# Optimization experiments

Measured on AMD Instinct MI355X. Metric: run time of the kernel, lower is better.

Reference implementation:

```python
import jax, jax.numpy as jnp
import numpy as np

N_NODES = 50000
N_EDGES = 800000
F_IN = 128
HIDDEN = 128
N_CLASSES = 40


def setup_inputs() -> dict:
    key = jax.random.key(0)
    k1, k2, k3, k4 = jax.random.split(key, 4)
    features = jax.random.normal(k1, (N_NODES, F_IN), dtype=jnp.float32)
    edge_index = jax.random.randint(k2, (2, N_EDGES), 0, N_NODES, dtype=jnp.int64)
    # Glorot-style init for the GCNConv linear weights, zero bias (PyG default)
    W1 = jax.random.normal(k3, (F_IN, HIDDEN), dtype=jnp.float32) * (1.0 / np.sqrt(F_IN))
    b1 = jnp.zeros((HIDDEN,), dtype=jnp.float32)
    W2 = jax.random.normal(k4, (HIDDEN, N_CLASSES), dtype=jnp.float32) * (1.0 / np.sqrt(HIDDEN))
    b2 = jnp.zeros((N_CLASSES,), dtype=jnp.float32)
    return {"features": features, "edge_index": edge_index,
            "W1": W1, "b1": b1, "W2": W2, "b2": b2}


def _gcn_norm(edge_index, num_nodes):
    # Add self-loops and compute symmetric normalization D^-1/2 (A+I) D^-1/2
    loop = jnp.arange(num_nodes, dtype=edge_index.dtype)
    src = jnp.concatenate([edge_index[0], loop])  # [E+N]
    dst = jnp.concatenate([edge_index[1], loop])  # [E+N]
    w = jnp.ones(src.shape[0], dtype=jnp.float32)
    deg = jax.ops.segment_sum(w, dst, num_segments=num_nodes)  # [N]
    dinv = jnp.where(deg > 0, jax.lax.rsqrt(deg), 0.0)
    norm = dinv[src] * w * dinv[dst]  # [E+N]
    return src, dst, norm


def _gcn_conv(x, W, b, src, dst, norm, num_nodes):
    h = x @ W  # linear transform first (PyG GCNConv): [N, out]
    msg = h[src] * norm[:, None]  # gather + scale: [E+N, out]
    out = jax.ops.segment_sum(msg, dst, num_segments=num_nodes)  # scatter-add
    return out + b


def reference(features, edge_index, W1, b1, W2, b2):
    n = features.shape[0]
    src, dst, norm = _gcn_norm(edge_index, n)
    x = jax.nn.relu(_gcn_conv(features, W1, b1, src, dst, norm, n))
    # dropout is identity at eval time (training=False)
    x = _gcn_conv(x, W2, b2, src, dst, norm, n)
    return jax.nn.log_softmax(x, axis=1)
```

## Files before the change

### kernel.cpp

```cpp
#include <hip/hip_runtime.h>
#include <hip/hip_bf16.h>
#include <math.h>

#define N_NODES 50000
#define N_EDGES 800000

#define SCAN_CHUNK 512
#define SCAN_NB ((N_NODES + SCAN_CHUNK - 1) / SCAN_CHUNK)

__global__ __launch_bounds__(256) void count_kernel(const int* __restrict__ ei,
                                                    int* __restrict__ cnt) {
  int e = blockIdx.x * 256 + threadIdx.x;
  if (e < N_EDGES) {
    int d = ei[N_EDGES + e];
    d = min(max(d, 0), N_NODES - 1);
    atomicAdd(&cnt[d], 1);
  }
}

__global__ __launch_bounds__(256) void scan_reduce(const int* __restrict__ cnt,
                                                   int* __restrict__ bsum) {
  __shared__ int s[256];
  int t = threadIdx.x;
  int i0 = blockIdx.x * SCAN_CHUNK + t * 2;
  int v = 0;
  if (i0 < N_NODES) v += cnt[i0];
  if (i0 + 1 < N_NODES) v += cnt[i0 + 1];
  s[t] = v;
  __syncthreads();
  for (int off = 128; off > 0; off >>= 1) {
    if (t < off) s[t] += s[t + off];
    __syncthreads();
  }
  if (t == 0) bsum[blockIdx.x] = s[0];
}

__global__ void scan_block(int* bsum) {
  __shared__ int s[128];
  int t = threadIdx.x;
  int v = (t < SCAN_NB) ? bsum[t] : 0;
  s[t] = v;
  __syncthreads();
  for (int off = 1; off < 128; off <<= 1) {
    int a = (t >= off) ? s[t - off] : 0;
    __syncthreads();
    s[t] += a;
    __syncthreads();
  }
  if (t < SCAN_NB) bsum[t] = s[t] - v;
}

__global__ __launch_bounds__(256) void scan_final(const int* __restrict__ cnt,
                                                  const int* __restrict__ bsum,
                                                  int* __restrict__ rowptr,
                                                  int* __restrict__ cursor,
                                                  float* __restrict__ dinv) {
  __shared__ int s[256];
  int t = threadIdx.x;
  int b = blockIdx.x;
  int i0 = b * SCAN_CHUNK + t * 2;
  int c0 = (i0 < N_NODES) ? cnt[i0] : 0;
  int c1 = (i0 + 1 < N_NODES) ? cnt[i0 + 1] : 0;
  int v = c0 + c1;
  s[t] = v;
  __syncthreads();
  for (int off = 1; off < 256; off <<= 1) {
    int a = (t >= off) ? s[t - off] : 0;
    __syncthreads();
    s[t] += a;
    __syncthreads();
  }
  int excl = s[t] - v + bsum[b];
  if (i0 < N_NODES) {
    rowptr[i0] = excl;
    cursor[i0] = excl;
    dinv[i0] = rsqrtf((float)(c0 + 1));
  }
  if (i0 + 1 < N_NODES) {
    rowptr[i0 + 1] = excl + c0;
    cursor[i0 + 1] = excl + c0;
    dinv[i0 + 1] = rsqrtf((float)(c1 + 1));
  }
  if (b == 0 && t == 0) rowptr[N_NODES] = N_EDGES;
}

__global__ __launch_bounds__(256) void fill_kernel(const int* __restrict__ ei,
                                                   int* __restrict__ cursor,
                                                   int* __restrict__ col) {
  int e = blockIdx.x * 256 + threadIdx.x;
  if (e >= N_EDGES) return;
  int srcv = ei[e];
  int dstv = ei[N_EDGES + e];
  srcv = min(max(srcv, 0), N_NODES - 1);
  dstv = min(max(dstv, 0), N_NODES - 1);
  int p = atomicAdd(&cursor[dstv], 1);
  col[p] = srcv;
}

__global__ __launch_bounds__(256) void gemm1_kernel(const float* __restrict__ X,
                                                    const float* __restrict__ W,
                                                    const float* __restrict__ dinv,
                                                    float* __restrict__ h1p) {
  __shared__ float xs[128 * 64];
  __shared__ float ws[128 * 64];
  int t = threadIdx.x;
  int row0 = blockIdx.x * 128;
  int wv = t >> 6, lane = t & 63;
  int wr = (wv >> 1) << 6, wc = (wv & 1) << 6;
  int tr = lane >> 3, tc = lane & 7;
  float acc[8][8];
#pragma unroll
  for (int i = 0; i < 8; ++i)
#pragma unroll
    for (int m = 0; m < 8; ++m) acc[i][m] = 0.f;

  for (int h = 0; h < 2; ++h) {
    if (h) __syncthreads();
#pragma unroll
    for (int it = 0; it < 8; ++it) {
      int idx = t + it * 256;
      int r = idx >> 4, kq = idx & 15;
      int gr = row0 + r;
      if (gr >= N_NODES) gr = N_NODES - 1;
      float4 v = *(const float4*)(X + (size_t)gr * 128 + h * 64 + kq * 4);
      *(float4*)(xs + r * 64 + ((kq ^ (r & 7)) << 2)) = v;
    }
#pragma unroll
    for (int it = 0; it < 8; ++it) {
      int idx = t + it * 256;
      int k = idx >> 5, jq = idx & 31;
      float4 v = *(const float4*)(W + (size_t)(h * 64 + k) * 128 + jq * 4);
      int kc = k >> 2, kr = k & 3;
      int j0 = jq * 4;
      ws[(j0 + 0) * 64 + (((kc ^ ((j0 + 0) & 7)) << 2) | kr)] = v.x;
      ws[(j0 + 1) * 64 + (((kc ^ ((j0 + 1) & 7)) << 2) | kr)] = v.y;
      ws[(j0 + 2) * 64 + (((kc ^ ((j0 + 2) & 7)) << 2) | kr)] = v.z;
      ws[(j0 + 3) * 64 + (((kc ^ ((j0 + 3) & 7)) << 2) | kr)] = v.w;
    }
    __syncthreads();
    for (int kq = 0; kq < 16; ++kq) {
      float4 xv[8], wvv[8];
#pragma unroll
      for (int i = 0; i < 8; ++i)
        xv[i] = *(const float4*)(xs + (wr + tr + 8 * i) * 64 + ((kq ^ tr) << 2));
#pragma unroll
      for (int m = 0; m < 8; ++m)
        wvv[m] = *(const float4*)(ws + (wc + tc + 8 * m) * 64 + ((kq ^ tc) << 2));
#pragma unroll
      for (int i = 0; i < 8; ++i)
#pragma unroll
        for (int m = 0; m < 8; ++m) {
          acc[i][m] = fmaf(xv[i].x, wvv[m].x, acc[i][m]);
          acc[i][m] = fmaf(xv[i].y, wvv[m].y, acc[i][m]);
          acc[i][m] = fmaf(xv[i].z, wvv[m].z, acc[i][m]);
          acc[i][m] = fmaf(xv[i].w, wvv[m].w, acc[i][m]);
        }
    }
  }
#pragma unroll
  for (int i = 0; i < 8; ++i) {
    int gr = row0 + wr + tr + 8 * i;
    if (gr < N_NODES) {
      float di = dinv[gr];
#pragma unroll
      for (int m = 0; m < 8; ++m)
        h1p[(size_t)gr * 128 + wc + tc + 8 * m] = di * acc[i][m];
    }
  }
}

__global__ __launch_bounds__(256) void agg1_kernel(const float* __restrict__ h1p,
                                                   const int* __restrict__ rowptr,
                                                   const int* __restrict__ col,
                                                   const float* __restrict__ dinv,
                                                   const float* __restrict__ b1,
                                                   float* __restrict__ x2) {
  int wid = (blockIdx.x * 256 + threadIdx.x) >> 6;
  int lane = threadIdx.x & 63;
  if (wid >= N_NODES) return;
  int rs = rowptr[wid], re = rowptr[wid + 1];
  int half = lane >> 5;
  int fl = lane & 31;
  const float4* hp4 = (const float4*)h1p;
  float4 z = {0.f, 0.f, 0.f, 0.f};
  float4 a0 = (half == 0) ? hp4[(size_t)wid * 32 + fl] : z;
  float4 a1 = z, a2 = z, a3 = z;
  for (int base = rs; base < re; base += 64) {
    int idx = base + lane;
    int c = (idx < re) ? col[idx] : 0;
    int nb = min(64, re - base);
    int e = 0;
    for (; e + 8 <= nb; e += 8) {
      int s0 = __shfl(c, e + half);
      int s1 = __shfl(c, e + 2 + half);
      int s2 = __shfl(c, e + 4 + half);
      int s3 = __shfl(c, e + 6 + half);
      float4 v0 = hp4[(size_t)s0 * 32 + fl];
      float4 v1 = hp4[(size_t)s1 * 32 + fl];
      float4 v2 = hp4[(size_t)s2 * 32 + fl];
      float4 v3 = hp4[(size_t)s3 * 32 + fl];
      a0.x += v0.x; a0.y += v0.y; a0.z += v0.z; a0.w += v0.w;
      a1.x += v1.x; a1.y += v1.y; a1.z += v1.z; a1.w += v1.w;
      a2.x += v2.x; a2.y += v2.y; a2.z += v2.z; a2.w += v2.w;
      a3.x += v3.x; a3.y += v3.y; a3.z += v3.z; a3.w += v3.w;
    }
    for (; e + 2 <= nb; e += 2) {
      int s0 = __shfl(c, e + half);
      float4 v0 = hp4[(size_t)s0 * 32 + fl];
      a0.x += v0.x; a0.y += v0.y; a0.z += v0.z; a0.w += v0.w;
    }
    if (e < nb) {
      int s0 = __shfl(c, e);
      if (half == 0) {
        float4 v0 = hp4[(size_t)s0 * 32 + fl];
        a0.x += v0.x; a0.y += v0.y; a0.z += v0.z; a0.w += v0.w;
      }
    }
  }
  float4 a;
  a.x = (a0.x + a1.x) + (a2.x + a3.x);
  a.y = (a0.y + a1.y) + (a2.y + a3.y);
  a.z = (a0.z + a1.z) + (a2.z + a3.z);
  a.w = (a0.w + a1.w) + (a2.w + a3.w);
  a.x += __shfl_xor(a.x, 32);
  a.y += __shfl_xor(a.y, 32);
  a.z += __shfl_xor(a.z, 32);
  a.w += __shfl_xor(a.w, 32);
  if (half == 0) {
    float di = dinv[wid];
    float4 bb = ((const float4*)b1)[fl];
    float4 o;
    o.x = fmaxf(fmaf(di, a.x, bb.x), 0.f);
    o.y = fmaxf(fmaf(di, a.y, bb.y), 0.f);
    o.z = fmaxf(fmaf(di, a.z, bb.z), 0.f);
    o.w = fmaxf(fmaf(di, a.w, bb.w), 0.f);
    *(float4*)(x2 + (size_t)wid * 128 + fl * 4) = o;
  }
}

__global__ __launch_bounds__(256) void gemm2_kernel(const float* __restrict__ X2,
                                                    const float* __restrict__ W2,
                                                    const float* __restrict__ dinv,
                                                    float* __restrict__ h2p) {
  __shared__ float xs[64 * 128];
  __shared__ float ws[40 * 128];
  int t = threadIdx.x;
  int row0 = blockIdx.x * 64;
#pragma unroll
  for (int it = 0; it < 8; ++it) {
    int idx = t + it * 256;
    int r = idx >> 5, kq = idx & 31;
    int gr = row0 + r;
    if (gr >= N_NODES) gr = N_NODES - 1;
    float4 v = *(const float4*)(X2 + (size_t)gr * 128 + kq * 4);
    *(float4*)(xs + r * 128 + ((kq ^ (r & 7)) << 2)) = v;
  }
  for (int idx = t; idx < 1280; idx += 256) {
    int k = idx / 10, jq = idx % 10;
    float4 v = *(const float4*)(W2 + k * 40 + jq * 4);
    int kc = k >> 2, kr = k & 3;
    int j0 = jq * 4;
    ws[(j0 + 0) * 128 + (((kc ^ ((j0 + 0) & 7)) << 2) | kr)] = v.x;
    ws[(j0 + 1) * 128 + (((kc ^ ((j0 + 1) & 7)) << 2) | kr)] = v.y;
    ws[(j0 + 2) * 128 + (((kc ^ ((j0 + 2) & 7)) << 2) | kr)] = v.z;
    ws[(j0 + 3) * 128 + (((kc ^ ((j0 + 3) & 7)) << 2) | kr)] = v.w;
  }
  __syncthreads();
  int wv = t >> 6, lane = t & 63;
  int tr = lane >> 3, tc = lane & 7;
  int rbase = wv * 16;
  float acc[2][5];
#pragma unroll
  for (int i = 0; i < 2; ++i)
#pragma unroll
    for (int m = 0; m < 5; ++m) acc[i][m] = 0.f;
  for (int kq = 0; kq < 32; ++kq) {
    float4 xv[2], wvv[5];
#pragma unroll
    for (int i = 0; i < 2; ++i)
      xv[i] = *(const float4*)(xs + (rbase + tr + 8 * i) * 128 + ((kq ^ tr) << 2));
#pragma unroll
    for (int m = 0; m < 5; ++m)
      wvv[m] = *(const float4*)(ws + (tc + 8 * m) * 128 + ((kq ^ tc) << 2));
#pragma unroll
    for (int i = 0; i < 2; ++i)
#pragma unroll
      for (int m = 0; m < 5; ++m) {
        acc[i][m] = fmaf(xv[i].x, wvv[m].x, acc[i][m]);
        acc[i][m] = fmaf(xv[i].y, wvv[m].y, acc[i][m]);
        acc[i][m] = fmaf(xv[i].z, wvv[m].z, acc[i][m]);
        acc[i][m] = fmaf(xv[i].w, wvv[m].w, acc[i][m]);
      }
  }
#pragma unroll
  for (int i = 0; i < 2; ++i) {
    int gr = row0 + rbase + tr + 8 * i;
    if (gr < N_NODES) {
      float di = dinv[gr];
#pragma unroll
      for (int m = 0; m < 5; ++m)
        h2p[(size_t)gr * 40 + tc + 8 * m] = di * acc[i][m];
    }
  }
}

__global__ __launch_bounds__(256) void agg2_softmax_kernel(const float* __restrict__ h2p,
                                                           const int* __restrict__ rowptr,
                                                           const int* __restrict__ col,
                                                           const float* __restrict__ dinv,
                                                           const float* __restrict__ b2,
                                                           float* __restrict__ out) {
  int wid = (blockIdx.x * 256 + threadIdx.x) >> 6;
  int lane = threadIdx.x & 63;
  if (wid >= N_NODES) return;
  int rs = rowptr[wid], re = rowptr[wid + 1];
  bool act = lane < 40;
  float ac0 = act ? h2p[(size_t)wid * 40 + lane] : 0.f;
  float ac1 = 0.f, ac2 = 0.f, ac3 = 0.f;
  for (int base = rs; base < re; base += 64) {
    int idx = base + lane;
    int c = (idx < re) ? col[idx] : 0;
    int nb = min(64, re - base);
    int e = 0;
    for (; e + 4 <= nb; e += 4) {
      int s0 = __shfl(c, e), s1 = __shfl(c, e + 1);
      int s2 = __shfl(c, e + 2), s3 = __shfl(c, e + 3);
      if (act) {
        ac0 += h2p[(size_t)s0 * 40 + lane];
        ac1 += h2p[(size_t)s1 * 40 + lane];
        ac2 += h2p[(size_t)s2 * 40 + lane];
        ac3 += h2p[(size_t)s3 * 40 + lane];
      }
    }
    for (; e < nb; ++e) {
      int s0 = __shfl(c, e);
      if (act) ac0 += h2p[(size_t)s0 * 40 + lane];
    }
  }
  float acc = (ac0 + ac1) + (ac2 + ac3);
  float v = act ? fmaf(dinv[wid], acc, b2[lane]) : -1e30f;
  float m = v;
#pragma unroll
  for (int off = 32; off > 0; off >>= 1) m = fmaxf(m, __shfl_xor(m, off));
  float ex = act ? expf(v - m) : 0.f;
  float ssum = ex;
#pragma unroll
  for (int off = 32; off > 0; off >>= 1) ssum += __shfl_xor(ssum, off);
  float ls = logf(ssum);
  if (act) out[(size_t)wid * 40 + lane] = v - m - ls;
}

extern "C" void kernel_launch(void* const* d_in, const int* in_sizes, int n_in,
                              void* d_out, int out_size, void* d_ws, size_t ws_size,
                              hipStream_t stream) {
  const float* X = (const float*)d_in[0];
  const int* ei = (const int*)d_in[1];
  const float* W1 = (const float*)d_in[2];
  const float* b1 = (const float*)d_in[3];
  const float* W2 = (const float*)d_in[4];
  const float* b2 = (const float*)d_in[5];
  float* out = (float*)d_out;

  char* p = (char*)d_ws;
  auto carve = [&](size_t bytes) -> void* {
    void* q = (void*)p;
    p += (bytes + 255) & ~(size_t)255;
    return q;
  };
  float* h1p = (float*)carve((size_t)N_NODES * 128 * 4);
  float* x2 = (float*)carve((size_t)N_NODES * 128 * 4);
  float* h2p = (float*)carve((size_t)N_NODES * 40 * 4);
  int* col = (int*)carve((size_t)N_EDGES * 4);
  int* cnt = (int*)carve((size_t)N_NODES * 4);
  int* rowptr = (int*)carve((size_t)(N_NODES + 1) * 4);
  int* cursor = (int*)carve((size_t)N_NODES * 4);
  float* dinv = (float*)carve((size_t)N_NODES * 4);
  int* bsum = (int*)carve((size_t)SCAN_NB * 4);

  hipMemsetAsync(cnt, 0, (size_t)N_NODES * 4, stream);
  count_kernel<<<(N_EDGES + 255) / 256, 256, 0, stream>>>(ei, cnt);
  scan_reduce<<<SCAN_NB, 256, 0, stream>>>(cnt, bsum);
  scan_block<<<1, 128, 0, stream>>>(bsum);
  scan_final<<<SCAN_NB, 256, 0, stream>>>(cnt, bsum, rowptr, cursor, dinv);
  fill_kernel<<<(N_EDGES + 255) / 256, 256, 0, stream>>>(ei, cursor, col);
  gemm1_kernel<<<(N_NODES + 127) / 128, 256, 0, stream>>>(X, W1, dinv, h1p);
  agg1_kernel<<<(N_NODES + 3) / 4, 256, 0, stream>>>(h1p, rowptr, col, dinv, b1, x2);
  gemm2_kernel<<<(N_NODES + 63) / 64, 256, 0, stream>>>(x2, W2, dinv, h2p);
  agg2_softmax_kernel<<<(N_NODES + 3) / 4, 256, 0, stream>>>(h2p, rowptr, col, dinv, b2, out);
}
```

Measured before the change: 314.4 us.

## Fuse CSR construction into one cooperative kernel and pad h2p rows to 48

Replaces the memset and the five CSR-building kernels (count, scan_reduce, scan_block, scan_final, fill) with one cooperative kernel of 256 blocks. Its phases are separated by grid-wide syncs, and the scan now covers one node per thread. This removes several launch gaps and the separate memset at the cost of grid-barrier overhead and fewer threads running the atomic count and fill loops. It also pads the layer-2 feature rows from 40 to 48 floats, so each gathered row starts on a 64-byte boundary and touches fewer cache lines during aggregation.

```diff
diff --git a/kernel.cpp b/kernel.cpp
--- a/kernel.cpp
+++ b/kernel.cpp
@@ -1,67 +1,40 @@
 #include <hip/hip_runtime.h>
 #include <hip/hip_bf16.h>
+#include <hip/hip_cooperative_groups.h>
 #include <math.h>
+
+namespace cg = cooperative_groups;
 
 #define N_NODES 50000
 #define N_EDGES 800000
 
-#define SCAN_CHUNK 512
-#define SCAN_NB ((N_NODES + SCAN_CHUNK - 1) / SCAN_CHUNK)
-
-__global__ __launch_bounds__(256) void count_kernel(const int* __restrict__ ei,
-                                                    int* __restrict__ cnt) {
-  int e = blockIdx.x * 256 + threadIdx.x;
-  if (e < N_EDGES) {
+#define CSR_NB 256
+
+__global__ __launch_bounds__(256) void coop_csr_kernel(const int* __restrict__ ei,
+                                                       int* __restrict__ cnt,
+                                                       int* __restrict__ bsum,
+                                                       int* __restrict__ rowptr,
+                                                       int* __restrict__ cursor,
+                                                       float* __restrict__ dinv,
+                                                       int* __restrict__ col) {
+  cg::grid_group grid = cg::this_grid();
+  __shared__ int s[256];
+  int t = threadIdx.x;
+  int bid = blockIdx.x;
+  int tid = bid * 256 + t;
+  const int NT = CSR_NB * 256;
+
+  for (int i = tid; i < N_NODES; i += NT) cnt[i] = 0;
+  grid.sync();
+
+  for (int e = tid; e < N_EDGES; e += NT) {
     int d = ei[N_EDGES + e];
     d = min(max(d, 0), N_NODES - 1);
     atomicAdd(&cnt[d], 1);
   }
-}
-
-__global__ __launch_bounds__(256) void scan_reduce(const int* __restrict__ cnt,
-                                                   int* __restrict__ bsum) {
-  __shared__ int s[256];
-  int t = threadIdx.x;
-  int i0 = blockIdx.x * SCAN_CHUNK + t * 2;
-  int v = 0;
-  if (i0 < N_NODES) v += cnt[i0];
-  if (i0 + 1 < N_NODES) v += cnt[i0 + 1];
-  s[t] = v;
-  __syncthreads();
-  for (int off = 128; off > 0; off >>= 1) {
-    if (t < off) s[t] += s[t + off];
-    __syncthreads();
-  }
-  if (t == 0) bsum[blockIdx.x] = s[0];
-}
-
-__global__ void scan_block(int* bsum) {
-  __shared__ int s[128];
-  int t = threadIdx.x;
-  int v = (t < SCAN_NB) ? bsum[t] : 0;
-  s[t] = v;
-  __syncthreads();
-  for (int off = 1; off < 128; off <<= 1) {
-    int a = (t >= off) ? s[t - off] : 0;
-    __syncthreads();
-    s[t] += a;
-    __syncthreads();
-  }
-  if (t < SCAN_NB) bsum[t] = s[t] - v;
-}
-
-__global__ __launch_bounds__(256) void scan_final(const int* __restrict__ cnt,
-                                                  const int* __restrict__ bsum,
-                                                  int* __restrict__ rowptr,
-                                                  int* __restrict__ cursor,
-                                                  float* __restrict__ dinv) {
-  __shared__ int s[256];
-  int t = threadIdx.x;
-  int b = blockIdx.x;
-  int i0 = b * SCAN_CHUNK + t * 2;
-  int c0 = (i0 < N_NODES) ? cnt[i0] : 0;
-  int c1 = (i0 + 1 < N_NODES) ? cnt[i0 + 1] : 0;
-  int v = c0 + c1;
+  grid.sync();
+
+  int v = (tid < N_NODES) ? cnt[tid] : 0;
   s[t] = v;
   __syncthreads();
   for (int off = 1; off < 256; off <<= 1) {
@@ -70,31 +43,42 @@
     s[t] += a;
     __syncthreads();
   }
-  int excl = s[t] - v + bsum[b];
-  if (i0 < N_NODES) {
-    rowptr[i0] = excl;
-    cursor[i0] = excl;
-    dinv[i0] = rsqrtf((float)(c0 + 1));
-  }
-  if (i0 + 1 < N_NODES) {
-    rowptr[i0 + 1] = excl + c0;
-    cursor[i0 + 1] = excl + c0;
-    dinv[i0 + 1] = rsqrtf((float)(c1 + 1));
-  }
-  if (b == 0 && t == 0) rowptr[N_NODES] = N_EDGES;
-}
-
-__global__ __launch_bounds__(256) void fill_kernel(const int* __restrict__ ei,
-                                                   int* __restrict__ cursor,
-                                                   int* __restrict__ col) {
-  int e = blockIdx.x * 256 + threadIdx.x;
-  if (e >= N_EDGES) return;
-  int srcv = ei[e];
-  int dstv = ei[N_EDGES + e];
-  srcv = min(max(srcv, 0), N_NODES - 1);
-  dstv = min(max(dstv, 0), N_NODES - 1);
-  int p = atomicAdd(&cursor[dstv], 1);
-  col[p] = srcv;
+  int incl = s[t];
+  int excl = incl - v;
+  if (t == 255) bsum[bid] = incl;
+  grid.sync();
+
+  if (bid == 0) {
+    int b = bsum[t];
+    s[t] = b;
+    __syncthreads();
+    for (int off = 1; off < 256; off <<= 1) {
+      int a = (t >= off) ? s[t - off] : 0;
+      __syncthreads();
+      s[t] += a;
+      __syncthreads();
+    }
+    bsum[t] = s[t] - b;
+  }
+  grid.sync();
+
+  if (tid < N_NODES) {
+    int e0 = excl + bsum[bid];
+    rowptr[tid] = e0;
+    cursor[tid] = e0;
+    dinv[tid] = rsqrtf((float)(v + 1));
+  }
+  if (tid == 0) rowptr[N_NODES] = N_EDGES;
+  grid.sync();
+
+  for (int e = tid; e < N_EDGES; e += NT) {
+    int srcv = ei[e];
+    int dstv = ei[N_EDGES + e];
+    srcv = min(max(srcv, 0), N_NODES - 1);
+    dstv = min(max(dstv, 0), N_NODES - 1);
+    int p = atomicAdd(&cursor[dstv], 1);
+    col[p] = srcv;
+  }
 }
 
 __global__ __launch_bounds__(256) void gemm1_kernel(const float* __restrict__ X,
@@ -299,7 +283,7 @@
       float di = dinv[gr];
 #pragma unroll
       for (int m = 0; m < 5; ++m)
-        h2p[(size_t)gr * 40 + tc + 8 * m] = di * acc[i][m];
+        h2p[(size_t)gr * 48 + tc + 8 * m] = di * acc[i][m];
     }
   }
 }
@@ -315,7 +299,7 @@
   if (wid >= N_NODES) return;
   int rs = rowptr[wid], re = rowptr[wid + 1];
   bool act = lane < 40;
-  float ac0 = act ? h2p[(size_t)wid * 40 + lane] : 0.f;
+  float ac0 = act ? h2p[(size_t)wid * 48 + lane] : 0.f;
   float ac1 = 0.f, ac2 = 0.f, ac3 = 0.f;
   for (int base = rs; base < re; base += 64) {
     int idx = base + lane;
@@ -326,15 +310,15 @@
       int s0 = __shfl(c, e), s1 = __shfl(c, e + 1);
       int s2 = __shfl(c, e + 2), s3 = __shfl(c, e + 3);
       if (act) {
-        ac0 += h2p[(size_t)s0 * 40 + lane];
-        ac1 += h2p[(size_t)s1 * 40 + lane];
-        ac2 += h2p[(size_t)s2 * 40 + lane];
-        ac3 += h2p[(size_t)s3 * 40 + lane];
+        ac0 += h2p[(size_t)s0 * 48 + lane];
+        ac1 += h2p[(size_t)s1 * 48 + lane];
+        ac2 += h2p[(size_t)s2 * 48 + lane];
+        ac3 += h2p[(size_t)s3 * 48 + lane];
       }
     }
     for (; e < nb; ++e) {
       int s0 = __shfl(c, e);
-      if (act) ac0 += h2p[(size_t)s0 * 40 + lane];
+      if (act) ac0 += h2p[(size_t)s0 * 48 + lane];
     }
   }
   float acc = (ac0 + ac1) + (ac2 + ac3);
@@ -369,20 +353,18 @@
   };
   float* h1p = (float*)carve((size_t)N_NODES * 128 * 4);
   float* x2 = (float*)carve((size_t)N_NODES * 128 * 4);
-  float* h2p = (float*)carve((size_t)N_NODES * 40 * 4);
+  float* h2p = (float*)carve((size_t)N_NODES * 48 * 4);
   int* col = (int*)carve((size_t)N_EDGES * 4);
   int* cnt = (int*)carve((size_t)N_NODES * 4);
   int* rowptr = (int*)carve((size_t)(N_NODES + 1) * 4);
   int* cursor = (int*)carve((size_t)N_NODES * 4);
   float* dinv = (float*)carve((size_t)N_NODES * 4);
-  int* bsum = (int*)carve((size_t)SCAN_NB * 4);
-
-  hipMemsetAsync(cnt, 0, (size_t)N_NODES * 4, stream);
-  count_kernel<<<(N_EDGES + 255) / 256, 256, 0, stream>>>(ei, cnt);
-  scan_reduce<<<SCAN_NB, 256, 0, stream>>>(cnt, bsum);
-  scan_block<<<1, 128, 0, stream>>>(bsum);
-  scan_final<<<SCAN_NB, 256, 0, stream>>>(cnt, bsum, rowptr, cursor, dinv);
-  fill_kernel<<<(N_EDGES + 255) / 256, 256, 0, stream>>>(ei, cursor, col);
+  int* bsum = (int*)carve((size_t)CSR_NB * 4);
+
+  void* csr_args[] = {(void*)&ei, (void*)&cnt, (void*)&bsum, (void*)&rowptr,
+                      (void*)&cursor, (void*)&dinv, (void*)&col};
+  hipLaunchCooperativeKernel((const void*)coop_csr_kernel, dim3(CSR_NB), dim3(256),
+                             csr_args, 0, stream);
   gemm1_kernel<<<(N_NODES + 127) / 128, 256, 0, stream>>>(X, W1, dinv, h1p);
   agg1_kernel<<<(N_NODES + 3) / 4, 256, 0, stream>>>(h1p, rowptr, col, dinv, b1, x2);
   gemm2_kernel<<<(N_NODES + 63) / 64, 256, 0, stream>>>(x2, W2, dinv, h2p);
```

New measurement: 469.0 us. +49.2%, slower.

## Store first-layer hidden features in bf16 and pad second-layer rows to 48

Applied to the files above, without the earlier changes.

The first GEMM now writes its normalized output as bf16, which halves the bytes the first aggregation gathers per neighbor. The aggregation kernel is restructured so each quarter-wave handles one neighbor row with 16 lanes loading 8 bf16 values each, and bf16 is unpacked to fp32 with shifts and masks before accumulating. The second-layer intermediate row stride is padded from 40 to 48 floats, which aligns gathered rows. Rounding to bf16 adds accuracy loss to the hidden activations.

```diff
diff --git a/kernel.cpp b/kernel.cpp
--- a/kernel.cpp
+++ b/kernel.cpp
@@ -100,7 +100,7 @@
 __global__ __launch_bounds__(256) void gemm1_kernel(const float* __restrict__ X,
                                                     const float* __restrict__ W,
                                                     const float* __restrict__ dinv,
-                                                    float* __restrict__ h1p) {
+                                                    __hip_bfloat16* __restrict__ h1p) {
   __shared__ float xs[128 * 64];
   __shared__ float ws[128 * 64];
   int t = threadIdx.x;
@@ -164,12 +164,12 @@
       float di = dinv[gr];
 #pragma unroll
       for (int m = 0; m < 8; ++m)
-        h1p[(size_t)gr * 128 + wc + tc + 8 * m] = di * acc[i][m];
-    }
-  }
-}
-
-__global__ __launch_bounds__(256) void agg1_kernel(const float* __restrict__ h1p,
+        h1p[(size_t)gr * 128 + wc + tc + 8 * m] = __float2bfloat16(di * acc[i][m]);
+    }
+  }
+}
+
+__global__ __launch_bounds__(256) void agg1_kernel(const __hip_bfloat16* __restrict__ h1p,
                                                    const int* __restrict__ rowptr,
                                                    const int* __restrict__ col,
                                                    const float* __restrict__ dinv,
@@ -179,62 +179,72 @@
   int lane = threadIdx.x & 63;
   if (wid >= N_NODES) return;
   int rs = rowptr[wid], re = rowptr[wid + 1];
-  int half = lane >> 5;
-  int fl = lane & 31;
-  const float4* hp4 = (const float4*)h1p;
-  float4 z = {0.f, 0.f, 0.f, 0.f};
-  float4 a0 = (half == 0) ? hp4[(size_t)wid * 32 + fl] : z;
-  float4 a1 = z, a2 = z, a3 = z;
+  int q = lane >> 4;
+  int fl = lane & 15;
+  const uint4* hp = (const uint4*)h1p;
+  float a0[8], a1[8];
+#pragma unroll
+  for (int j = 0; j < 8; ++j) { a0[j] = 0.f; a1[j] = 0.f; }
+
+#define ACC_BF16(A, U)                                                        \
+  {                                                                           \
+    uint4 u_ = (U);                                                           \
+    A[0] += __uint_as_float(u_.x << 16);                                      \
+    A[1] += __uint_as_float(u_.x & 0xffff0000u);                              \
+    A[2] += __uint_as_float(u_.y << 16);                                      \
+    A[3] += __uint_as_float(u_.y & 0xffff0000u);                              \
+    A[4] += __uint_as_float(u_.z << 16);                                      \
+    A[5] += __uint_as_float(u_.z & 0xffff0000u);                              \
+    A[6] += __uint_as_float(u_.w << 16);                                      \
+    A[7] += __uint_as_float(u_.w & 0xffff0000u);                              \
+  }
+
+  if (q == 0) ACC_BF16(a0, hp[(size_t)wid * 16 + fl]);
+
   for (int base = rs; base < re; base += 64) {
     int idx = base + lane;
     int c = (idx < re) ? col[idx] : 0;
     int nb = min(64, re - base);
     int e = 0;
     for (; e + 8 <= nb; e += 8) {
-      int s0 = __shfl(c, e + half);
-      int s1 = __shfl(c, e + 2 + half);
-      int s2 = __shfl(c, e + 4 + half);
-      int s3 = __shfl(c, e + 6 + half);
-      float4 v0 = hp4[(size_t)s0 * 32 + fl];
-      float4 v1 = hp4[(size_t)s1 * 32 + fl];
-      float4 v2 = hp4[(size_t)s2 * 32 + fl];
-      float4 v3 = hp4[(size_t)s3 * 32 + fl];
-      a0.x += v0.x; a0.y += v0.y; a0.z += v0.z; a0.w += v0.w;
-      a1.x += v1.x; a1.y += v1.y; a1.z += v1.z; a1.w += v1.w;
-      a2.x += v2.x; a2.y += v2.y; a2.z += v2.z; a2.w += v2.w;
-      a3.x += v3.x; a3.y += v3.y; a3.z += v3.z; a3.w += v3.w;
-    }
-    for (; e + 2 <= nb; e += 2) {
-      int s0 = __shfl(c, e + half);
-      float4 v0 = hp4[(size_t)s0 * 32 + fl];
-      a0.x += v0.x; a0.y += v0.y; a0.z += v0.z; a0.w += v0.w;
-    }
-    if (e < nb) {
-      int s0 = __shfl(c, e);
-      if (half == 0) {
-        float4 v0 = hp4[(size_t)s0 * 32 + fl];
-        a0.x += v0.x; a0.y += v0.y; a0.z += v0.z; a0.w += v0.w;
+      int s0 = __shfl(c, e + q);
+      int s1 = __shfl(c, e + 4 + q);
+      uint4 u0 = hp[(size_t)s0 * 16 + fl];
+      uint4 u1 = hp[(size_t)s1 * 16 + fl];
+      ACC_BF16(a0, u0);
+      ACC_BF16(a1, u1);
+    }
+    for (; e < nb; e += 4) {
+      if (e + q < nb) {
+        int s0 = __shfl(c, e + q);
+        ACC_BF16(a0, hp[(size_t)s0 * 16 + fl]);
       }
     }
   }
-  float4 a;
-  a.x = (a0.x + a1.x) + (a2.x + a3.x);
-  a.y = (a0.y + a1.y) + (a2.y + a3.y);
-  a.z = (a0.z + a1.z) + (a2.z + a3.z);
-  a.w = (a0.w + a1.w) + (a2.w + a3.w);
-  a.x += __shfl_xor(a.x, 32);
-  a.y += __shfl_xor(a.y, 32);
-  a.z += __shfl_xor(a.z, 32);
-  a.w += __shfl_xor(a.w, 32);
-  if (half == 0) {
+#undef ACC_BF16
+
+#pragma unroll
+  for (int j = 0; j < 8; ++j) {
+    float v = a0[j] + a1[j];
+    v += __shfl_xor(v, 16);
+    v += __shfl_xor(v, 32);
+    a0[j] = v;
+  }
+  if (q == 0) {
     float di = dinv[wid];
-    float4 bb = ((const float4*)b1)[fl];
-    float4 o;
-    o.x = fmaxf(fmaf(di, a.x, bb.x), 0.f);
-    o.y = fmaxf(fmaf(di, a.y, bb.y), 0.f);
-    o.z = fmaxf(fmaf(di, a.z, bb.z), 0.f);
-    o.w = fmaxf(fmaf(di, a.w, bb.w), 0.f);
-    *(float4*)(x2 + (size_t)wid * 128 + fl * 4) = o;
+    float4 bb0 = ((const float4*)b1)[fl * 2];
+    float4 bb1 = ((const float4*)b1)[fl * 2 + 1];
+    float4 o0, o1;
+    o0.x = fmaxf(fmaf(di, a0[0], bb0.x), 0.f);
+    o0.y = fmaxf(fmaf(di, a0[1], bb0.y), 0.f);
+    o0.z = fmaxf(fmaf(di, a0[2], bb0.z), 0.f);
+    o0.w = fmaxf(fmaf(di, a0[3], bb0.w), 0.f);
+    o1.x = fmaxf(fmaf(di, a0[4], bb1.x), 0.f);
+    o1.y = fmaxf(fmaf(di, a0[5], bb1.y), 0.f);
+    o1.z = fmaxf(fmaf(di, a0[6], bb1.z), 0.f);
+    o1.w = fmaxf(fmaf(di, a0[7], bb1.w), 0.f);
+    *(float4*)(x2 + (size_t)wid * 128 + fl * 8) = o0;
+    *(float4*)(x2 + (size_t)wid * 128 + fl * 8 + 4) = o1;
   }
 }
 
@@ -299,7 +309,7 @@
       float di = dinv[gr];
 #pragma unroll
       for (int m = 0; m < 5; ++m)
-        h2p[(size_t)gr * 40 + tc + 8 * m] = di * acc[i][m];
+        h2p[(size_t)gr * 48 + tc + 8 * m] = di * acc[i][m];
     }
   }
 }
@@ -315,7 +325,7 @@
   if (wid >= N_NODES) return;
   int rs = rowptr[wid], re = rowptr[wid + 1];
   bool act = lane < 40;
-  float ac0 = act ? h2p[(size_t)wid * 40 + lane] : 0.f;
+  float ac0 = act ? h2p[(size_t)wid * 48 + lane] : 0.f;
   float ac1 = 0.f, ac2 = 0.f, ac3 = 0.f;
   for (int base = rs; base < re; base += 64) {
     int idx = base + lane;
@@ -326,15 +336,15 @@
       int s0 = __shfl(c, e), s1 = __shfl(c, e + 1);
       int s2 = __shfl(c, e + 2), s3 = __shfl(c, e + 3);
       if (act) {
-        ac0 += h2p[(size_t)s0 * 40 + lane];
-        ac1 += h2p[(size_t)s1 * 40 + lane];
-        ac2 += h2p[(size_t)s2 * 40 + lane];
-        ac3 += h2p[(size_t)s3 * 40 + lane];
+        ac0 += h2p[(size_t)s0 * 48 + lane];
+        ac1 += h2p[(size_t)s1 * 48 + lane];
+        ac2 += h2p[(size_t)s2 * 48 + lane];
+        ac3 += h2p[(size_t)s3 * 48 + lane];
       }
     }
     for (; e < nb; ++e) {
       int s0 = __shfl(c, e);
-      if (act) ac0 += h2p[(size_t)s0 * 40 + lane];
+      if (act) ac0 += h2p[(size_t)s0 * 48 + lane];
     }
   }
   float acc = (ac0 + ac1) + (ac2 + ac3);
@@ -367,9 +377,9 @@
     p += (bytes + 255) & ~(size_t)255;
     return q;
   };
-  float* h1p = (float*)carve((size_t)N_NODES * 128 * 4);
+  __hip_bfloat16* h1p = (__hip_bfloat16*)carve((size_t)N_NODES * 128 * 2);
   float* x2 = (float*)carve((size_t)N_NODES * 128 * 4);
-  float* h2p = (float*)carve((size_t)N_NODES * 40 * 4);
+  float* h2p = (float*)carve((size_t)N_NODES * 48 * 4);
   int* col = (int*)carve((size_t)N_EDGES * 4);
   int* cnt = (int*)carve((size_t)N_NODES * 4);
   int* rowptr = (int*)carve((size_t)(N_NODES + 1) * 4);
```

Measured after the change: 296.2 us. 1.06x faster.
